# Performance work log

Hardware: AMD Instinct MI355X
Metric: run time of the kernel (lower is better)

The kernel has to match this reference:

```python
import jax, jax.numpy as jnp
import numpy as np

B, Hh, Ww, C, HEADS, WS, SHIFT = 8, 64, 64, 768, 12, 8, 4
N = WS * WS
HID = 4 * C


def _rel_pos_index(ws):
    coords = np.stack(np.meshgrid(np.arange(ws), np.arange(ws), indexing='ij'))  # (2, ws, ws)
    cf = coords.reshape(2, -1)
    rel = (cf[:, :, None] - cf[:, None, :]).transpose(1, 2, 0)  # (N, N, 2)
    rel[:, :, 0] += ws - 1
    rel[:, :, 1] += ws - 1
    rel[:, :, 0] *= 2 * ws - 1
    return rel.sum(-1)  # (N, N) in [0, (2ws-1)^2)


def _attn_mask(Hp, Wp, ws, shift):
    # Standard Swin shifted-window attention mask: 0 within region, -100 across.
    img = np.zeros((Hp, Wp), dtype=np.float32)
    cnt = 0
    sls = (slice(0, -ws), slice(-ws, -shift), slice(-shift, None))
    for hs in sls:
        for wsl in sls:
            img[hs, wsl] = cnt
            cnt += 1
    w = img.reshape(Hp // ws, ws, Wp // ws, ws).transpose(0, 2, 1, 3).reshape(-1, ws * ws)
    diff = w[:, None, :] - w[:, :, None]
    return np.where(diff != 0, -100.0, 0.0).astype(np.float32)  # (nW, N, N)


def setup_inputs() -> dict:
    key = jax.random.key(0)
    ks = jax.random.split(key, 8)
    s = 0.02
    return {
        'x': jax.random.normal(ks[0], (B, Hh * Ww, C), jnp.float32),
        'c': jax.random.normal(ks[1], (B, C), jnp.float32),
        'mask_matrix': jnp.asarray(_attn_mask(Hh, Ww, WS, SHIFT)),
        'rel_index': jnp.asarray(_rel_pos_index(WS), dtype=jnp.int32),
        'w_adaln': jax.random.normal(ks[2], (C, 6 * C), jnp.float32) * s,
        'b_adaln': jnp.zeros((6 * C,), jnp.float32),
        'w_qkv': jax.random.normal(ks[3], (C, 3 * C), jnp.float32) * s,
        'b_qkv': jnp.zeros((3 * C,), jnp.float32),
        'rpb_table': jax.random.normal(ks[4], ((2 * WS - 1) ** 2, HEADS), jnp.float32) * s,
        'w_proj': jax.random.normal(ks[5], (C, C), jnp.float32) * s,
        'b_proj': jnp.zeros((C,), jnp.float32),
        'w_fc1': jax.random.normal(ks[6], (C, HID), jnp.float32) * s,
        'b_fc1': jnp.zeros((HID,), jnp.float32),
        'w_fc2': jax.random.normal(ks[7], (HID, C), jnp.float32) * s,
        'b_fc2': jnp.zeros((C,), jnp.float32),
        'H': Hh,
        'W': Ww,
    }


def _ln(x, eps=1e-6):
    # LayerNorm without affine params (elementwise_affine=False)
    mu = x.mean(-1, keepdims=True)
    var = x.var(-1, keepdims=True)
    return (x - mu) * jax.lax.rsqrt(var + eps)


def _modulate(x, shift, scale):
    return x * (1.0 + scale[:, None, :]) + shift[:, None, :]


def reference(x, c, mask_matrix, rel_index, w_adaln, b_adaln, w_qkv, b_qkv,
              rpb_table, w_proj, b_proj, w_fc1, b_fc1, w_fc2, b_fc2, H, W):
    Bb, L, Cc = x.shape
    hd = Cc // HEADS
    mod = jax.nn.silu(c) @ w_adaln + b_adaln  # (B, 6C)
    sh_msa, sc_msa, g_msa, sh_mlp, sc_mlp, g_mlp = jnp.split(mod, 6, axis=1)

    shortcut = x
    h = _modulate(_ln(x), sh_msa, sc_msa).reshape(Bb, H, W, Cc)
    # H,W are multiples of WS -> no padding; shift_size>0 -> roll + mask
    h = jnp.roll(h, (-SHIFT, -SHIFT), axis=(1, 2))
    nWh, nWw = H // WS, W // WS
    win = h.reshape(Bb, nWh, WS, nWw, WS, Cc).transpose(0, 1, 3, 2, 4, 5).reshape(-1, N, Cc)

    qkv = (win @ w_qkv + b_qkv).reshape(-1, N, 3, HEADS, hd).transpose(2, 0, 3, 1, 4)
    q = qkv[0] * (hd ** -0.5)
    k, v = qkv[1], qkv[2]
    attn = jnp.einsum('bhnd,bhmd->bhnm', q, k)  # (B_, heads, N, N)
    bias = rpb_table[rel_index.reshape(-1)].reshape(N, N, HEADS).transpose(2, 0, 1)
    attn = attn + bias[None]
    nW = mask_matrix.shape[0]
    attn = attn.reshape(Bb, nW, HEADS, N, N) + mask_matrix[None, :, None]
    attn = jax.nn.softmax(attn.reshape(-1, HEADS, N, N), axis=-1)
    out = jnp.einsum('bhnm,bhmd->bnhd', attn, v).reshape(-1, N, Cc)
    out = out @ w_proj + b_proj

    out = out.reshape(Bb, nWh, nWw, WS, WS, Cc).transpose(0, 1, 3, 2, 4, 5).reshape(Bb, H, W, Cc)
    out = jnp.roll(out, (SHIFT, SHIFT), axis=(1, 2)).reshape(Bb, L, Cc)

    x1 = shortcut + g_msa[:, None, :] * out
    h2 = _modulate(_ln(x1), sh_mlp, sc_mlp)
    mlp = jax.nn.gelu(h2 @ w_fc1 + b_fc1, approximate=False) @ w_fc2 + b_fc2
    return x1 + g_mlp[:, None, :] * mlp
```

## Files before the change

### kernel.cpp

```cpp
#include <hip/hip_runtime.h>
#include <hip/hip_bf16.h>
#include <math.h>

using bf16 = __hip_bfloat16;
using short8  = __attribute__((ext_vector_type(8))) short;
using floatx4 = __attribute__((ext_vector_type(4))) float;

__device__ __forceinline__ float b2f(bf16 v){ return __bfloat162float(v); }
__device__ __forceinline__ bf16  f2b(float v){ return __float2bfloat16(v); }
__device__ __forceinline__ float loadf(const void* p, size_t i, bool f32){
    return f32 ? ((const float*)p)[i] : b2f(((const bf16*)p)[i]);
}
__device__ __forceinline__ void gload16(const void* g, void* l){
    __builtin_amdgcn_global_load_lds(
        (const __attribute__((address_space(1))) unsigned int*)g,
        (__attribute__((address_space(3))) unsigned int*)l, 16, 0, 0);
}
__device__ __forceinline__ void bar(){
    asm volatile("" ::: "memory");
    __builtin_amdgcn_s_barrier();
    asm volatile("" ::: "memory");
}
template<int Nn> __device__ __forceinline__ void vmwait(){
    if constexpr (Nn == 0)      asm volatile("s_waitcnt vmcnt(0)" ::: "memory");
    else if constexpr (Nn == 3) asm volatile("s_waitcnt vmcnt(3)" ::: "memory");
    else                        asm volatile("s_waitcnt vmcnt(4)" ::: "memory");
}
__device__ __forceinline__ void lgkm0_fence(){
    asm volatile("s_waitcnt lgkmcnt(0)" ::: "memory");
    __builtin_amdgcn_sched_barrier(0);
}

#define FIXED_WS 14303488

__global__ void detect_k(const void* __restrict__ x, int* __restrict__ flag){
    __shared__ int cnt;
    if (threadIdx.x == 0) cnt = 0;
    __syncthreads();
    const unsigned short* u = (const unsigned short*)x;
    int local = 0;
    #pragma unroll
    for (int i = 0; i < 16; ++i){
        unsigned int w = u[threadIdx.x * 16 + i];
        float v = __uint_as_float(w << 16);
        float a = fabsf(v);
        if (!(a <= 1e4f) || (v != 0.f && a < 1e-20f)) local++;
    }
    atomicAdd(&cnt, local);
    __syncthreads();
    if (threadIdx.x == 0) *flag = (cnt > 200) ? 1 : 0;
}

__global__ void transpose_k(const void* __restrict__ W, bf16* __restrict__ WT, int K, int N,
                            const int* __restrict__ dflag){
    const bool f32 = (*dflag != 0);
    __shared__ bf16 t[32][33];
    int k0 = blockIdx.y * 32, n0 = blockIdx.x * 32;
    int tx = threadIdx.x, ty = threadIdx.y;
    #pragma unroll
    for (int r = ty; r < 32; r += 8) t[r][tx] = f2b(loadf(W, (size_t)(k0 + r) * N + n0 + tx, f32));
    __syncthreads();
    #pragma unroll
    for (int r = ty; r < 32; r += 8) WT[(size_t)(n0 + r) * K + k0 + tx] = t[tx][r];
}

__global__ __launch_bounds__(256) void adaln_k(const void* __restrict__ c, const void* __restrict__ w,
                                               const void* __restrict__ bv, float* __restrict__ mod,
                                               const int* __restrict__ dflag){
    const bool f32 = (*dflag != 0);
    int b = blockIdx.y;
    int jl = threadIdx.x & 63;
    int part = threadIdx.x >> 6;
    int j = blockIdx.x * 64 + jl;
    __shared__ float sc[768];
    for (int k = threadIdx.x; k < 768; k += 256){
        float v = loadf(c, b * 768 + k, f32);
        sc[k] = v / (1.f + __expf(-v));
    }
    __syncthreads();
    float acc = 0.f;
    int k0 = part * 192;
    #pragma unroll 4
    for (int k = k0; k < k0 + 192; ++k) acc += sc[k] * loadf(w, (size_t)k * 4608 + j, f32);
    __shared__ float red[4][64];
    red[part][jl] = acc;
    __syncthreads();
    if (part == 0)
        mod[b * 4608 + j] = red[0][jl] + red[1][jl] + red[2][jl] + red[3][jl] + loadf(bv, j, f32);
}

__device__ __forceinline__ float2 block_reduce_sum2(float s, float s2){
    #pragma unroll
    for (int m = 32; m >= 1; m >>= 1){
        s  += __shfl_xor(s,  m, 64);
        s2 += __shfl_xor(s2, m, 64);
    }
    __shared__ float red[8];
    int wave = threadIdx.x >> 6;
    if ((threadIdx.x & 63) == 0){ red[wave] = s; red[4 + wave] = s2; }
    __syncthreads();
    return make_float2(red[0] + red[1] + red[2] + red[3],
                       red[4] + red[5] + red[6] + red[7]);
}

__global__ __launch_bounds__(256) void ln_mod_win_k(const void* __restrict__ x, const float* __restrict__ mod,
                                                    bf16* __restrict__ win, int roff,
                                                    const int* __restrict__ dflag){
    const bool f32 = (*dflag != 0);
    int r = roff + blockIdx.x;
    int bw = r >> 6, n = r & 63;
    int b = bw >> 6, widx = bw & 63;
    int hh = (((widx >> 3) << 3) + (n >> 3) + 4) & 63;
    int ww = (((widx & 7) << 3) + (n & 7) + 4) & 63;
    size_t xo = ((size_t)b * 4096 + hh * 64 + ww) * 768;
    int t = threadIdx.x;
    float v0 = loadf(x, xo + t, f32), v1 = loadf(x, xo + t + 256, f32), v2 = loadf(x, xo + t + 512, f32);
    float2 ss = block_reduce_sum2(v0 + v1 + v2, v0 * v0 + v1 * v1 + v2 * v2);
    float mu = ss.x * (1.f / 768.f);
    float rstd = rsqrtf(ss.y * (1.f / 768.f) - mu * mu + 1e-6f);
    const float* mb = mod + b * 4608;
    bf16* wr = win + (size_t)blockIdx.x * 768;
    wr[t]       = f2b((v0 - mu) * rstd * (1.f + mb[768 + t])       + mb[t]);
    wr[t + 256] = f2b((v1 - mu) * rstd * (1.f + mb[768 + t + 256]) + mb[t + 256]);
    wr[t + 512] = f2b((v2 - mu) * rstd * (1.f + mb[768 + t + 512]) + mb[t + 512]);
}

__global__ __launch_bounds__(256) void ln_mod2_k(const void* __restrict__ x1, const float* __restrict__ mod,
                                                 bf16* __restrict__ h2, int roff,
                                                 const int* __restrict__ dflag){
    const bool f32 = (*dflag != 0);
    int t0 = roff + blockIdx.x;
    int b = t0 >> 12;
    size_t xo = (size_t)t0 * 768;
    int t = threadIdx.x;
    float v0 = loadf(x1, xo + t, f32), v1 = loadf(x1, xo + t + 256, f32), v2 = loadf(x1, xo + t + 512, f32);
    float2 ss = block_reduce_sum2(v0 + v1 + v2, v0 * v0 + v1 * v1 + v2 * v2);
    float mu = ss.x * (1.f / 768.f);
    float rstd = rsqrtf(ss.y * (1.f / 768.f) - mu * mu + 1e-6f);
    const float* mb = mod + b * 4608;
    bf16* wr = h2 + (size_t)blockIdx.x * 768;
    wr[t]       = f2b((v0 - mu) * rstd * (1.f + mb[3072 + t])       + mb[2304 + t]);
    wr[t + 256] = f2b((v1 - mu) * rstd * (1.f + mb[3072 + t + 256]) + mb[2304 + t + 256]);
    wr[t + 512] = f2b((v2 - mu) * rstd * (1.f + mb[3072 + t + 512]) + mb[2304 + t + 512]);
}

__global__ __launch_bounds__(256) void attn_k(const bf16* __restrict__ qkv, const void* __restrict__ maskm,
                                              const int* __restrict__ rel, const void* __restrict__ rpb,
                                              bf16* __restrict__ ao, int woff,
                                              const int* __restrict__ dflag){
    const bool f32 = (*dflag != 0);
    __shared__ bf16  qs[64][68];
    __shared__ float ks[64][65];
    __shared__ bf16  vs[64][64];
    __shared__ float Ps[64][68];
    int blk = blockIdx.x;
    int head = blk % 12;
    int bw = blk / 12;
    int tid = threadIdx.x;
    const bf16* base = qkv + (size_t)bw * 64 * 2304 + head * 64;
    for (int e4 = tid; e4 < 1024; e4 += 256){
        int n = e4 >> 4, d4 = (e4 & 15) * 4;
        size_t o = (size_t)n * 2304 + d4;
        ushort4 qv = *(const ushort4*)(base + o);
        ushort4 kv = *(const ushort4*)(base + o + 768);
        ushort4 vv = *(const ushort4*)(base + o + 1536);
        bf16 q0, q1, q2, q3;
        *(unsigned short*)&q0 = qv.x; *(unsigned short*)&q1 = qv.y;
        *(unsigned short*)&q2 = qv.z; *(unsigned short*)&q3 = qv.w;
        qs[n][d4]     = f2b(b2f(q0) * 0.125f);
        qs[n][d4 + 1] = f2b(b2f(q1) * 0.125f);
        qs[n][d4 + 2] = f2b(b2f(q2) * 0.125f);
        qs[n][d4 + 3] = f2b(b2f(q3) * 0.125f);
        bf16 k0, k1, k2, k3;
        *(unsigned short*)&k0 = kv.x; *(unsigned short*)&k1 = kv.y;
        *(unsigned short*)&k2 = kv.z; *(unsigned short*)&k3 = kv.w;
        ks[n][d4]     = b2f(k0); ks[n][d4 + 1] = b2f(k1);
        ks[n][d4 + 2] = b2f(k2); ks[n][d4 + 3] = b2f(k3);
        *(ushort4*)&vs[n][d4] = vv;
    }
    __syncthreads();
    size_t mo = (size_t)((woff + bw) & 63) * 4096;
    int i0 = (tid >> 4) * 4, j0 = (tid & 15) * 4;
    {
        float acc[4][4];
        #pragma unroll
        for (int a = 0; a < 4; ++a)
            #pragma unroll
            for (int b2 = 0; b2 < 4; ++b2) acc[a][b2] = 0.f;
        #pragma unroll 8
        for (int d = 0; d < 64; ++d){
            float qv[4], kv[4];
            #pragma unroll
            for (int a = 0; a < 4; ++a) qv[a] = b2f(qs[i0 + a][d]);
            #pragma unroll
            for (int b2 = 0; b2 < 4; ++b2) kv[b2] = ks[j0 + b2][d];
            #pragma unroll
            for (int a = 0; a < 4; ++a)
                #pragma unroll
                for (int b2 = 0; b2 < 4; ++b2) acc[a][b2] += qv[a] * kv[b2];
        }
        #pragma unroll
        for (int a = 0; a < 4; ++a){
            int i = i0 + a;
            int4 r4 = *(const int4*)&rel[i * 64 + j0];
            float4 o4;
            o4.x = acc[a][0] + loadf(rpb, (size_t)r4.x * 12 + head, f32) + loadf(maskm, mo + i * 64 + j0,     f32);
            o4.y = acc[a][1] + loadf(rpb, (size_t)r4.y * 12 + head, f32) + loadf(maskm, mo + i * 64 + j0 + 1, f32);
            o4.z = acc[a][2] + loadf(rpb, (size_t)r4.z * 12 + head, f32) + loadf(maskm, mo + i * 64 + j0 + 2, f32);
            o4.w = acc[a][3] + loadf(rpb, (size_t)r4.w * 12 + head, f32) + loadf(maskm, mo + i * 64 + j0 + 3, f32);
            *(float4*)&Ps[i][j0] = o4;
        }
    }
    __syncthreads();
    {
        int row = tid >> 2, p0 = (tid & 3) * 16;
        float mx = -1e30f;
        #pragma unroll
        for (int j = 0; j < 16; ++j) mx = fmaxf(mx, Ps[row][p0 + j]);
        mx = fmaxf(mx, __shfl_xor(mx, 1, 64));
        mx = fmaxf(mx, __shfl_xor(mx, 2, 64));
        float sum = 0.f;
        float ev[16];
        #pragma unroll
        for (int j = 0; j < 16; ++j){ ev[j] = __expf(Ps[row][p0 + j] - mx); sum += ev[j]; }
        sum += __shfl_xor(sum, 1, 64);
        sum += __shfl_xor(sum, 2, 64);
        float inv = 1.f / sum;
        #pragma unroll
        for (int j = 0; j < 16; ++j) Ps[row][p0 + j] = ev[j] * inv;
    }
    __syncthreads();
    {
        int d0 = j0;
        float po[4][4];
        #pragma unroll
        for (int a = 0; a < 4; ++a)
            #pragma unroll
            for (int b2 = 0; b2 < 4; ++b2) po[a][b2] = 0.f;
        #pragma unroll 8
        for (int j = 0; j < 64; ++j){
            float pv[4];
            #pragma unroll
            for (int a = 0; a < 4; ++a) pv[a] = Ps[i0 + a][j];
            ushort4 v4 = *(const ushort4*)&vs[j][d0];
            bf16 w0, w1, w2, w3;
            *(unsigned short*)&w0 = v4.x; *(unsigned short*)&w1 = v4.y;
            *(unsigned short*)&w2 = v4.z; *(unsigned short*)&w3 = v4.w;
            float vv[4] = {b2f(w0), b2f(w1), b2f(w2), b2f(w3)};
            #pragma unroll
            for (int a = 0; a < 4; ++a)
                #pragma unroll
                for (int b2 = 0; b2 < 4; ++b2) po[a][b2] += pv[a] * vv[b2];
        }
        #pragma unroll
        for (int a = 0; a < 4; ++a){
            ushort4 s4;
            bf16 t0 = f2b(po[a][0]), t1 = f2b(po[a][1]), t2 = f2b(po[a][2]), t3 = f2b(po[a][3]);
            s4.x = *(unsigned short*)&t0; s4.y = *(unsigned short*)&t1;
            s4.z = *(unsigned short*)&t2; s4.w = *(unsigned short*)&t3;
            *(ushort4*)&ao[((size_t)bw * 64 + i0 + a) * 768 + head * 64 + d0] = s4;
        }
    }
}

template<int EPI, int BN>
__global__ __launch_bounds__(256, (BN == 128) ? 3 : 4)
void gemm_k(const bf16* __restrict__ A, const bf16* __restrict__ BT,
            const void* __restrict__ bias, void* __restrict__ Cout,
            int N, int K, int roff,
            const void* __restrict__ xres, const float* __restrict__ mod,
            const void* __restrict__ x1,
            const int* __restrict__ dflag, int nMB, int total){
    constexpr int MFR = (BN == 128) ? 4 : 2;
    constexpr int LPT = (BN == 128) ? 4 : 3;
    const bool f32 = (*dflag != 0);
    __shared__ __align__(16) bf16 As[3][128 * 32];
    __shared__ __align__(16) bf16 Bs[3][BN * 32];

    int tid = threadIdx.x;
    int wave = tid >> 6, lane = tid & 63;
    int wm = (BN == 128) ? (wave >> 1) * 64 : wave * 32;
    int wn = (BN == 128) ? (wave & 1) * 64 : 0;
    int lrow = lane & 15, lq = lane >> 4;

    int G = (int)gridDim.x, bid = (int)blockIdx.x;
    int q = total / G, r = total % G;
    int myLen = q + (bid < r ? 1 : 0);
    int first = bid * q + (bid < r ? bid : r);
    const int nkt = K >> 5;
    int TS = myLen * nkt;

    int sc8 = ((((lane & 3) - ((lane >> 3) & 3)) & 3)) * 8;
    int srw = lane >> 2;
    int lofsA0 = (wave * 32) * 32;
    int lofsA1 = (wave * 32 + 16) * 32;
    int lofsB  = (BN == 128) ? lofsA0 : (wave * 16) * 32;
    int wB     = (BN == 128) ? wave * 32 : wave * 16;

    int fsw = ((lq + ((lrow >> 1) & 3)) & 3) * 8;
    int aoff = (wm + lrow) * 32 + fsw;
    int boff = (wn + lrow) * 32 + fsw;

    floatx4 acc[MFR][4];
    #pragma unroll
    for (int i = 0; i < MFR; ++i)
        #pragma unroll
        for (int j = 0; j < 4; ++j) acc[i][j] = floatx4{0.f, 0.f, 0.f, 0.f};

    int sIdx = first, sT = 0;
    const bf16 *gA, *gB;
    auto setPtrs = [&](){
        int m0s = (sIdx % nMB) * 128;
        int n0s = (sIdx / nMB) * BN;
        gA = A  + (size_t)(m0s + wave * 32 + srw) * K + sc8;
        gB = BT + (size_t)(n0s + wB + srw) * K + sc8;
    };
    setPtrs();
    auto stageStep = [&](int buf){
        size_t kof = (size_t)sT * 32;
        gload16(gA + kof,                  As[buf] + lofsA0);
        gload16(gA + kof + (size_t)16 * K, As[buf] + lofsA1);
        gload16(gB + kof,                  Bs[buf] + lofsB);
        if constexpr (BN == 128)
            gload16(gB + kof + (size_t)16 * K, Bs[buf] + lofsA1);
        if (++sT == nkt){ sT = 0; ++sIdx; setPtrs(); }
    };

    stageStep(0); stageStep(1);
    vmwait<LPT>();
    bar();

    int rIdx = first, rT = 0;
    int rm0 = (rIdx % nMB) * 128, rn0 = (rIdx / nMB) * BN;
    float bb[4];
    int bN0 = -1;
    int cur = 0, nx2 = 2;

    for (int T = 0; T < TS; ++T){
        short8 af[MFR], bfr[4];
        #pragma unroll
        for (int f = 0; f < MFR; ++f) af[f]  = *(const short8*)(As[cur] + aoff + f * 512);
        #pragma unroll
        for (int f = 0; f < 4;   ++f) bfr[f] = *(const short8*)(Bs[cur] + boff + f * 512);
        bool more = (T + 2 < TS);
        if (more) stageStep(nx2);
        lgkm0_fence();
        __builtin_amdgcn_s_setprio(1);
        #pragma unroll
        for (int mf = 0; mf < MFR; ++mf)
            #pragma unroll
            for (int nf = 0; nf < 4; ++nf)
                acc[mf][nf] = __builtin_amdgcn_mfma_f32_16x16x32_bf16(af[mf], bfr[nf], acc[mf][nf], 0, 0, 0);
        __builtin_amdgcn_s_setprio(0);
        if (T + 1 < TS){
            if (more) vmwait<LPT>();
            else      vmwait<0>();
            bar();
        }
        cur = (cur == 2) ? 0 : cur + 1;
        nx2 = (nx2 == 2) ? 0 : nx2 + 1;
        if (++rT == nkt){
            rT = 0;
            if (rn0 != bN0){
                bN0 = rn0;
                #pragma unroll
                for (int nf = 0; nf < 4; ++nf) bb[nf] = loadf(bias, rn0 + wn + nf * 16 + lrow, f32);
            }
            #pragma unroll
            for (int mf = 0; mf < MFR; ++mf){
                #pragma unroll
                for (int nf = 0; nf < 4; ++nf){
                    #pragma unroll
                    for (int rr = 0; rr < 4; ++rr){
                        int grow = rm0 + wm + mf * 16 + lq * 4 + rr;
                        int gcol = rn0 + wn + nf * 16 + lrow;
                        float v = acc[mf][nf][rr] + bb[nf];
                        if (EPI == 0){
                            ((bf16*)Cout)[(size_t)grow * N + gcol] = f2b(v);
                        } else if (EPI == 1){
                            float g = 0.5f * v * (1.f + erff(v * 0.70710678118654752f));
                            ((bf16*)Cout)[(size_t)grow * N + gcol] = f2b(g);
                        } else if (EPI == 2){
                            int gr = roff + grow;
                            int bw = gr >> 6, n = gr & 63;
                            int b = bw >> 6, widx = bw & 63;
                            int hh = (((widx >> 3) << 3) + (n >> 3) + 4) & 63;
                            int ww = (((widx & 7) << 3) + (n & 7) + 4) & 63;
                            size_t t = ((size_t)b * 4096 + hh * 64 + ww) * 768 + gcol;
                            float gm = mod[b * 4608 + 1536 + gcol];
                            float res = loadf(xres, t, f32) + gm * v;
                            if (f32) ((float*)Cout)[t] = res; else ((bf16*)Cout)[t] = f2b(res);
                        } else {
                            int gr = roff + grow;
                            int b = gr >> 12;
                            float gm = mod[b * 4608 + 3840 + gcol];
                            size_t t = (size_t)gr * N + gcol;
                            float res = loadf(x1, t, f32) + gm * v;
                            if (f32) ((float*)Cout)[t] = res; else ((bf16*)Cout)[t] = f2b(res);
                        }
                    }
                }
            }
            #pragma unroll
            for (int i = 0; i < MFR; ++i)
                #pragma unroll
                for (int j = 0; j < 4; ++j) acc[i][j] = floatx4{0.f, 0.f, 0.f, 0.f};
            ++rIdx;
            rm0 = (rIdx % nMB) * 128; rn0 = (rIdx / nMB) * BN;
        }
    }
}

extern "C" void kernel_launch(void* const* d_in, const int* in_sizes, int n_in,
                              void* d_out, int out_size, void* d_ws, size_t ws_size,
                              hipStream_t stream){
    const void* x       = d_in[0];
    const void* c       = d_in[1];
    const void* maskm   = d_in[2];
    const int*  rel     = (const int*)d_in[3];
    const void* w_adaln = d_in[4];
    const void* b_adaln = d_in[5];
    const void* w_qkv   = d_in[6];
    const void* b_qkv   = d_in[7];
    const void* rpb     = d_in[8];
    const void* w_proj  = d_in[9];
    const void* b_proj  = d_in[10];
    const void* w_fc1   = d_in[11];
    const void* b_fc1   = d_in[12];
    const void* w_fc2   = d_in[13];
    const void* b_fc2   = d_in[14];

    int Mc = 4096;
    for (int cand = 8192; cand >= 256; cand >>= 1){
        if (FIXED_WS + (size_t)cand * 7680u <= ws_size){ Mc = cand; break; }
    }
    int Mc2 = Mc;
    if (FIXED_WS + 16384ull * 7680u <= ws_size && Mc == 8192) Mc2 = 16384;
    const int nc   = 32768 / Mc;
    const int nc2  = 32768 / Mc2;
    const int nMB  = Mc  / 128;
    const int nMB2 = Mc2 / 128;
    const int McF  = (Mc2 > 8192) ? 8192 : Mc2;
    const int nMBF = McF / 128;

    char* ws = (char*)d_ws;
    int*  dflag  = (int*)(ws);
    float* mod   = (float*)(ws + 256);
    bf16* wqkvT  = (bf16*)(ws + 147712);
    bf16* wprojT = (bf16*)(ws + 3686656);
    bf16* wfc1T  = (bf16*)(ws + 4866304);
    bf16* wfc2T  = (bf16*)(ws + 9584896);
    bf16* win_c  = (bf16*)(ws + FIXED_WS);
    bf16* big_c  = (bf16*)(ws + FIXED_WS + (size_t)Mc * 1536);
    bf16* ao_c   = (bf16*)(ws + FIXED_WS + (size_t)Mc * 6144);
    bf16* h2_c   = (bf16*)(ws + FIXED_WS);
    bf16* fc1o_c = (bf16*)(ws + FIXED_WS + (size_t)Mc2 * 1536);
    void* x1     = d_out;
    void* out    = d_out;

    detect_k<<<1, 256, 0, stream>>>(x, dflag);

    dim3 tb(32, 8);
    transpose_k<<<dim3(2304/32, 768/32),  tb, 0, stream>>>(w_qkv,  wqkvT,  768, 2304, dflag);
    transpose_k<<<dim3(768/32,  768/32),  tb, 0, stream>>>(w_proj, wprojT, 768, 768, dflag);
    transpose_k<<<dim3(3072/32, 768/32),  tb, 0, stream>>>(w_fc1,  wfc1T,  768, 3072, dflag);
    transpose_k<<<dim3(768/32,  3072/32), tb, 0, stream>>>(w_fc2,  wfc2T,  3072, 768, dflag);
    adaln_k<<<dim3(72, 8), 256, 0, stream>>>(c, w_adaln, b_adaln, mod, dflag);

    const int G128 = 768;
    const int G64  = 1024;
    for (int ch = 0; ch < nc; ++ch){
        int roff = ch * Mc;
        ln_mod_win_k<<<Mc, 256, 0, stream>>>(x, mod, win_c, roff, dflag);
        int tqkv = nMB * 18;
        gemm_k<0,128><<<(tqkv < G128 ? tqkv : G128), 256, 0, stream>>>(win_c, wqkvT, b_qkv, big_c,
                                                    2304, 768, 0, nullptr, nullptr, nullptr, dflag, nMB, tqkv);
        attn_k<<<(Mc/64) * 12, 256, 0, stream>>>(big_c, maskm, rel, rpb, ao_c, roff / 64, dflag);
        int tproj = nMB * 12;
        gemm_k<2,64><<<(tproj < G64 ? tproj : G64), 256, 0, stream>>>(ao_c, wprojT, b_proj, x1,
                                                   768, 768, roff, x, mod, nullptr, dflag, nMB, tproj);
    }
    for (int ch = 0; ch < nc2; ++ch){
        int roff = ch * Mc2;
        ln_mod2_k<<<Mc2, 256, 0, stream>>>(x1, mod, h2_c, roff, dflag);
        int tfc1 = nMB2 * 24;
        gemm_k<1,128><<<(tfc1 < G128 ? tfc1 : G128), 256, 0, stream>>>(h2_c, wfc1T, b_fc1, fc1o_c,
                                                    3072, 768, 0, nullptr, nullptr, nullptr, dflag, nMB2, tfc1);
        for (int sub = 0; sub < Mc2 / McF; ++sub){
            int tfc2 = nMBF * 12;
            gemm_k<3,64><<<(tfc2 < G64 ? tfc2 : G64), 256, 0, stream>>>(
                fc1o_c + (size_t)sub * McF * 3072, wfc2T, b_fc2, out,
                768, 3072, roff + sub * McF, nullptr, mod, x1, dflag, nMBF, tfc2);
        }
    }
}
```

Measured before the change: 1.204 ms.

## Use MFMA bf16 instructions for window attention QK^T and PV products

Replaces the scalar FP32 outer-product loops in the attention kernel with 16x16x32 bf16 MFMA instructions for both the score and output matmuls. Q, K, V^T and the softmax probabilities are stored in LDS as swizzled bf16 tiles so that lanes can load MFMA fragments without bank conflicts. This is meant to cut ALU time in the attention stage. In exchange, probabilities are rounded to bf16 before PV, the bias and mask adds become scalar gathers, and output stores are no longer vectorised.

```diff
diff --git a/kernel.cpp b/kernel.cpp
--- a/kernel.cpp
+++ b/kernel.cpp
@@ -149,13 +149,13 @@
                                               bf16* __restrict__ ao, int woff,
                                               const int* __restrict__ dflag){
     const bool f32 = (*dflag != 0);
-    __shared__ bf16  qs[64][68];
-    __shared__ float ks[64][65];
-    __shared__ bf16  vs[64][64];
+    __shared__ __align__(16) bf16 qs[2 * 64 * 32];
+    __shared__ __align__(16) bf16 kb[2 * 64 * 32];
+    __shared__ __align__(16) bf16 vt[2 * 64 * 32];
+    __shared__ __align__(16) bf16 Pb[2 * 64 * 32];
     __shared__ float Ps[64][68];
-    int blk = blockIdx.x;
-    int head = blk % 12;
-    int bw = blk / 12;
+    int head = blockIdx.x % 12;
+    int bw = blockIdx.x / 12;
     int tid = threadIdx.x;
     const bf16* base = qkv + (size_t)bw * 64 * 2304 + head * 64;
     for (int e4 = tid; e4 < 1024; e4 += 256){
@@ -167,49 +167,53 @@
         bf16 q0, q1, q2, q3;
         *(unsigned short*)&q0 = qv.x; *(unsigned short*)&q1 = qv.y;
         *(unsigned short*)&q2 = qv.z; *(unsigned short*)&q3 = qv.w;
-        qs[n][d4]     = f2b(b2f(q0) * 0.125f);
-        qs[n][d4 + 1] = f2b(b2f(q1) * 0.125f);
-        qs[n][d4 + 2] = f2b(b2f(q2) * 0.125f);
-        qs[n][d4 + 3] = f2b(b2f(q3) * 0.125f);
-        bf16 k0, k1, k2, k3;
-        *(unsigned short*)&k0 = kv.x; *(unsigned short*)&k1 = kv.y;
-        *(unsigned short*)&k2 = kv.z; *(unsigned short*)&k3 = kv.w;
-        ks[n][d4]     = b2f(k0); ks[n][d4 + 1] = b2f(k1);
-        ks[n][d4 + 2] = b2f(k2); ks[n][d4 + 3] = b2f(k3);
-        *(ushort4*)&vs[n][d4] = vv;
-    }
-    __syncthreads();
+        q0 = f2b(b2f(q0) * 0.125f); q1 = f2b(b2f(q1) * 0.125f);
+        q2 = f2b(b2f(q2) * 0.125f); q3 = f2b(b2f(q3) * 0.125f);
+        ushort4 qsc;
+        qsc.x = *(unsigned short*)&q0; qsc.y = *(unsigned short*)&q1;
+        qsc.z = *(unsigned short*)&q2; qsc.w = *(unsigned short*)&q3;
+        int h = d4 >> 5, e = d4 & 31;
+        int off = (((e >> 3) + ((n >> 1) & 3)) & 3) * 8 + (e & 7);
+        *(ushort4*)&qs[(h * 64 + n) * 32 + off] = qsc;
+        *(ushort4*)&kb[(h * 64 + n) * 32 + off] = kv;
+        int hv = n >> 5, ev_ = n & 31;
+        int cv = ev_ >> 3;
+        unsigned short vb[4] = {vv.x, vv.y, vv.z, vv.w};
+        #pragma unroll
+        for (int j = 0; j < 4; ++j){
+            int dr = d4 + j;
+            int slot = (cv + ((dr >> 1) & 3)) & 3;
+            *((unsigned short*)&vt[(hv * 64 + dr) * 32 + slot * 8 + (ev_ & 7)]) = vb[j];
+        }
+    }
+    __syncthreads();
+    int lane = tid & 63, w = tid >> 6;
+    int lrow = lane & 15, lq = lane >> 4;
     size_t mo = (size_t)((woff + bw) & 63) * 4096;
-    int i0 = (tid >> 4) * 4, j0 = (tid & 15) * 4;
+    int arow = w * 16 + lrow;
+    int asw = ((lq + ((lrow >> 1) & 3)) & 3) * 8;
     {
-        float acc[4][4];
-        #pragma unroll
-        for (int a = 0; a < 4; ++a)
-            #pragma unroll
-            for (int b2 = 0; b2 < 4; ++b2) acc[a][b2] = 0.f;
-        #pragma unroll 8
-        for (int d = 0; d < 64; ++d){
-            float qv[4], kv[4];
-            #pragma unroll
-            for (int a = 0; a < 4; ++a) qv[a] = b2f(qs[i0 + a][d]);
-            #pragma unroll
-            for (int b2 = 0; b2 < 4; ++b2) kv[b2] = ks[j0 + b2][d];
-            #pragma unroll
-            for (int a = 0; a < 4; ++a)
-                #pragma unroll
-                for (int b2 = 0; b2 < 4; ++b2) acc[a][b2] += qv[a] * kv[b2];
-        }
-        #pragma unroll
-        for (int a = 0; a < 4; ++a){
-            int i = i0 + a;
-            int4 r4 = *(const int4*)&rel[i * 64 + j0];
-            float4 o4;
-            o4.x = acc[a][0] + loadf(rpb, (size_t)r4.x * 12 + head, f32) + loadf(maskm, mo + i * 64 + j0,     f32);
-            o4.y = acc[a][1] + loadf(rpb, (size_t)r4.y * 12 + head, f32) + loadf(maskm, mo + i * 64 + j0 + 1, f32);
-            o4.z = acc[a][2] + loadf(rpb, (size_t)r4.z * 12 + head, f32) + loadf(maskm, mo + i * 64 + j0 + 2, f32);
-            o4.w = acc[a][3] + loadf(rpb, (size_t)r4.w * 12 + head, f32) + loadf(maskm, mo + i * 64 + j0 + 3, f32);
-            *(float4*)&Ps[i][j0] = o4;
-        }
+        floatx4 sacc[4];
+        #pragma unroll
+        for (int jt = 0; jt < 4; ++jt) sacc[jt] = floatx4{0.f, 0.f, 0.f, 0.f};
+        #pragma unroll
+        for (int ksl = 0; ksl < 2; ++ksl){
+            short8 aq = *(const short8*)&qs[(ksl * 64 + arow) * 32 + asw];
+            #pragma unroll
+            for (int jt = 0; jt < 4; ++jt){
+                short8 bk = *(const short8*)&kb[(ksl * 64 + jt * 16 + lrow) * 32 + asw];
+                sacc[jt] = __builtin_amdgcn_mfma_f32_16x16x32_bf16(aq, bk, sacc[jt], 0, 0, 0);
+            }
+        }
+        #pragma unroll
+        for (int jt = 0; jt < 4; ++jt)
+            #pragma unroll
+            for (int rr = 0; rr < 4; ++rr){
+                int i = w * 16 + lq * 4 + rr, j = jt * 16 + lrow;
+                Ps[i][j] = sacc[jt][rr]
+                         + loadf(rpb, (size_t)rel[i * 64 + j] * 12 + head, f32)
+                         + loadf(maskm, mo + i * 64 + j, f32);
+            }
     }
     __syncthreads();
     {
@@ -226,40 +230,41 @@
         sum += __shfl_xor(sum, 1, 64);
         sum += __shfl_xor(sum, 2, 64);
         float inv = 1.f / sum;
-        #pragma unroll
-        for (int j = 0; j < 16; ++j) Ps[row][p0 + j] = ev[j] * inv;
+        int h = p0 >> 5, e0 = p0 & 31;
+        int rsw = (row >> 1) & 3;
+        #pragma unroll
+        for (int g = 0; g < 2; ++g){
+            int slot = (((e0 >> 3) + g) + rsw) & 3;
+            short8 pk;
+            #pragma unroll
+            for (int j = 0; j < 8; ++j){
+                bf16 t = f2b(ev[g * 8 + j] * inv);
+                pk[j] = *(short*)&t;
+            }
+            *(short8*)&Pb[(h * 64 + row) * 32 + slot * 8] = pk;
+        }
     }
     __syncthreads();
     {
-        int d0 = j0;
-        float po[4][4];
-        #pragma unroll
-        for (int a = 0; a < 4; ++a)
-            #pragma unroll
-            for (int b2 = 0; b2 < 4; ++b2) po[a][b2] = 0.f;
-        #pragma unroll 8
-        for (int j = 0; j < 64; ++j){
-            float pv[4];
-            #pragma unroll
-            for (int a = 0; a < 4; ++a) pv[a] = Ps[i0 + a][j];
-            ushort4 v4 = *(const ushort4*)&vs[j][d0];
-            bf16 w0, w1, w2, w3;
-            *(unsigned short*)&w0 = v4.x; *(unsigned short*)&w1 = v4.y;
-            *(unsigned short*)&w2 = v4.z; *(unsigned short*)&w3 = v4.w;
-            float vv[4] = {b2f(w0), b2f(w1), b2f(w2), b2f(w3)};
-            #pragma unroll
-            for (int a = 0; a < 4; ++a)
-                #pragma unroll
-                for (int b2 = 0; b2 < 4; ++b2) po[a][b2] += pv[a] * vv[b2];
-        }
-        #pragma unroll
-        for (int a = 0; a < 4; ++a){
-            ushort4 s4;
-            bf16 t0 = f2b(po[a][0]), t1 = f2b(po[a][1]), t2 = f2b(po[a][2]), t3 = f2b(po[a][3]);
-            s4.x = *(unsigned short*)&t0; s4.y = *(unsigned short*)&t1;
-            s4.z = *(unsigned short*)&t2; s4.w = *(unsigned short*)&t3;
-            *(ushort4*)&ao[((size_t)bw * 64 + i0 + a) * 768 + head * 64 + d0] = s4;
-        }
+        floatx4 oacc[4];
+        #pragma unroll
+        for (int dt = 0; dt < 4; ++dt) oacc[dt] = floatx4{0.f, 0.f, 0.f, 0.f};
+        #pragma unroll
+        for (int ksl = 0; ksl < 2; ++ksl){
+            short8 ap = *(const short8*)&Pb[(ksl * 64 + arow) * 32 + asw];
+            #pragma unroll
+            for (int dt = 0; dt < 4; ++dt){
+                short8 bv2 = *(const short8*)&vt[(ksl * 64 + dt * 16 + lrow) * 32 + asw];
+                oacc[dt] = __builtin_amdgcn_mfma_f32_16x16x32_bf16(ap, bv2, oacc[dt], 0, 0, 0);
+            }
+        }
+        #pragma unroll
+        for (int dt = 0; dt < 4; ++dt)
+            #pragma unroll
+            for (int rr = 0; rr < 4; ++rr){
+                int i = w * 16 + lq * 4 + rr, d = dt * 16 + lrow;
+                ao[((size_t)bw * 64 + i) * 768 + head * 64 + d] = f2b(oacc[dt][rr]);
+            }
     }
 }
 
```

After: 1.154 ms. 4.2% less time.
